# Performance work log

Hardware: AMD Instinct MI355X
Metric: run time of the kernel (lower is better)

Reference implementation:

```python
import jax, jax.numpy as jnp
import numpy as np

N_NODES = 100000
N_EDGES = 800000
NODE_IN = 32
EDGE_DIM = 84
HIDDEN = 24
HEAD_HIDDEN = 20
DEPTH = 2
CAT = 2 * HIDDEN + EDGE_DIM  # 132
LN_EPS = 1e-5


def _gelu(x):
    # torch nn.GELU default = exact erf form
    return jax.nn.gelu(x, approximate=False)


def _ln(x, g, b):
    m = jnp.mean(x, axis=-1, keepdims=True)
    v = jnp.var(x, axis=-1, keepdims=True)
    return (x - m) * jax.lax.rsqrt(v + LN_EPS) * g + b


def setup_inputs() -> dict:
    key = jax.random.key(0)
    ks = jax.random.split(key, 32)
    f = jnp.float32

    def nrm(k, shape, scale=0.05):
        return jax.random.normal(k, shape, dtype=f) * scale

    inp = {
        "x": jax.random.normal(ks[0], (N_NODES, NODE_IN), dtype=f),
        "edge_attr": jax.random.normal(ks[1], (N_EDGES, EDGE_DIM), dtype=f),
        # input projection
        "node_w": nrm(ks[2], (NODE_IN, HIDDEN)),
        "node_b": jnp.zeros((HIDDEN,), f),
        # intrinsic head
        "ih_w1": nrm(ks[3], (HIDDEN, HEAD_HIDDEN)),
        "ih_b1": jnp.zeros((HEAD_HIDDEN,), f),
        "ih_w2": nrm(ks[4], (HEAD_HIDDEN, 1)),
        "ih_b2": jnp.zeros((1,), f),
        # per-layer phi_e (stacked over depth)
        "pe_w1": nrm(ks[5], (DEPTH, CAT, EDGE_DIM)),
        "pe_b1": jnp.zeros((DEPTH, EDGE_DIM), f),
        "pe_w2": nrm(ks[6], (DEPTH, EDGE_DIM, EDGE_DIM)),
        "pe_b2": jnp.zeros((DEPTH, EDGE_DIM), f),
        # per-layer phi_v
        "pv_w1": nrm(ks[7], (DEPTH, CAT, HIDDEN)),
        "pv_b1": jnp.zeros((DEPTH, HIDDEN), f),
        "pv_w2": nrm(ks[8], (DEPTH, HIDDEN, HIDDEN)),
        "pv_b2": jnp.zeros((DEPTH, HIDDEN), f),
        # layer norms
        "ne_g": jnp.ones((DEPTH, EDGE_DIM), f),
        "ne_b": jnp.zeros((DEPTH, EDGE_DIM), f),
        "nv_g": jnp.ones((DEPTH, HIDDEN), f),
        "nv_b": jnp.zeros((DEPTH, HIDDEN), f),
        # context head
        "ch_w1": nrm(ks[9], (HIDDEN, HEAD_HIDDEN)),
        "ch_b1": jnp.zeros((HEAD_HIDDEN,), f),
        "ch_w2": nrm(ks[10], (HEAD_HIDDEN, 1)),
        "ch_b2": jnp.zeros((1,), f),
        "mu": jnp.zeros((), f),
        "edge_index": jax.random.randint(ks[11], (2, N_EDGES), 0, N_NODES),
    }
    return inp


def reference(x, edge_attr, node_w, node_b, ih_w1, ih_b1, ih_w2, ih_b2,
              pe_w1, pe_b1, pe_w2, pe_b2, pv_w1, pv_b1, pv_w2, pv_b2,
              ne_g, ne_b, nv_g, nv_b, ch_w1, ch_b1, ch_w2, ch_b2, mu,
              edge_index):
    src, dst = edge_index[0], edge_index[1]
    n = x.shape[0]
    # eval mode: dropout and edge_drop are inactive
    h = x @ node_w + node_b                                   # [N, H]
    intrinsic = (_gelu(h @ ih_w1 + ih_b1) @ ih_w2 + ih_b2)[:, 0]
    e = edge_attr                                             # [E, De]
    ones = jnp.ones((src.shape[0], 1), dtype=x.dtype)
    counts = jnp.maximum(jax.ops.segment_sum(ones, dst, num_segments=n), 1.0)
    for i in range(DEPTH):
        hs, hd = h[src], h[dst]                               # gathers [E, H]
        cat = jnp.concatenate([hs, hd, e], axis=-1)           # [E, 132]
        e_msg = _gelu(cat @ pe_w1[i] + pe_b1[i]) @ pe_w2[i] + pe_b2[i]
        e = _ln(e + e_msg, ne_g[i], ne_b[i])
        cat = jnp.concatenate([hs, hd, e], axis=-1)
        m = _gelu(cat @ pv_w1[i] + pv_b1[i]) @ pv_w2[i] + pv_b2[i]
        agg = jax.ops.segment_sum(m, dst, num_segments=n) / counts  # scatter-mean
        h = _ln(h + agg, nv_g[i], nv_b[i])
    context = (_gelu(h @ ch_w1 + ch_b1) @ ch_w2 + ch_b2)[:, 0]
    return mu + intrinsic + context
```

## Files before the change

### kernel.cpp

```cpp
#include <hip/hip_runtime.h>
#include <math.h>

#define N_NODES 100000
#define N_EDGES 800000
#define NODE_IN 32
#define EDGE_DIM 84
#define HIDDEN 24
#define HEAD_HIDDEN 20
#define CAT_DIM 132
#define LN_EPS 1e-5f

typedef __attribute__((ext_vector_type(8))) short short8;
typedef __attribute__((ext_vector_type(4))) short bfx4;
typedef __attribute__((ext_vector_type(4))) float f32x4;
typedef unsigned int uint;
typedef unsigned short ushort;

__device__ __forceinline__ float gelu_exact(float x) {
    return 0.5f * x * (1.0f + erff(x * 0.70710678118654752f));
}
__device__ __forceinline__ ushort f2bf(float f) {
    union { float f; uint u; } c; c.f = f;
    uint u = c.u;
    return (ushort)((u + 0x7fffu + ((u >> 16) & 1u)) >> 16);
}
__device__ __forceinline__ float bf2f(ushort s) {
    union { uint u; float f; } c; c.u = ((uint)s) << 16; return c.f;
}

__global__ void k_prep_w(const float* __restrict__ pe_w1, const float* __restrict__ pe_w2,
                         const float* __restrict__ pv_w1, const float* __restrict__ pv_w2,
                         ushort* __restrict__ wp) {
    int idx = blockIdx.x * 256 + threadIdx.x;
    int j = idx & 7;
    int lane = (idx >> 3) & 63;
    int frag = idx >> 9;
    int kq = (lane >> 4) * 8 + j;
    int n15 = lane & 15;
    float v = 0.f;
    if (frag < 60) {
        int l = frag / 30, f = frag % 30;
        int kt = f / 6, nt = f % 6;
        int k = kt * 32 + kq, n = nt * 16 + n15;
        if (k < CAT_DIM && n < EDGE_DIM) v = pe_w1[(l * CAT_DIM + k) * EDGE_DIM + n];
    } else if (frag < 96) {
        int f2 = frag - 60; int l = f2 / 18, f = f2 % 18;
        int kt = f / 6, nt = f % 6;
        int k = kt * 32 + kq, n = nt * 16 + n15;
        if (k < EDGE_DIM && n < EDGE_DIM) v = pe_w2[(l * EDGE_DIM + k) * EDGE_DIM + n];
    } else if (frag < 116) {
        int f2 = frag - 96; int l = f2 / 10, f = f2 % 10;
        int kt = f / 2, nt = f % 2;
        int k = kt * 32 + kq, n = nt * 16 + n15;
        if (k < CAT_DIM && n < HIDDEN) v = pv_w1[(l * CAT_DIM + k) * HIDDEN + n];
    } else {
        int f2 = frag - 116; int l = f2 / 2, nt = f2 % 2;
        int k = kq, n = nt * 16 + n15;
        if (k < HIDDEN && n < HIDDEN) v = pv_w2[(l * HIDDEN + k) * HIDDEN + n];
    }
    wp[idx] = f2bf(v);
}

__global__ void k_node_in(const float* __restrict__ x,
                          const float* __restrict__ node_w, const float* __restrict__ node_b,
                          const float* __restrict__ ih_w1, const float* __restrict__ ih_b1,
                          const float* __restrict__ ih_w2, const float* __restrict__ ih_b2,
                          float* __restrict__ h, ushort* __restrict__ h_bf,
                          float* __restrict__ intr) {
    int n = blockIdx.x * blockDim.x + threadIdx.x;
    if (n >= N_NODES) return;
    float xv[NODE_IN];
    const float4* xp = (const float4*)(x + (size_t)n * NODE_IN);
#pragma unroll
    for (int i = 0; i < NODE_IN / 4; i++) {
        float4 v = xp[i];
        xv[4*i+0] = v.x; xv[4*i+1] = v.y; xv[4*i+2] = v.z; xv[4*i+3] = v.w;
    }
    float hv[HIDDEN];
#pragma unroll
    for (int j = 0; j < HIDDEN; j++) hv[j] = node_b[j];
    for (int k = 0; k < NODE_IN; k++) {
        float xk = xv[k];
#pragma unroll
        for (int j = 0; j < HIDDEN; j++) hv[j] = fmaf(xk, node_w[k * HIDDEN + j], hv[j]);
    }
#pragma unroll
    for (int j = 0; j < HIDDEN; j++) {
        h[(size_t)n * HIDDEN + j] = hv[j];
        h_bf[(size_t)n * HIDDEN + j] = f2bf(hv[j]);
    }
    float acc = ih_b2[0];
    for (int j = 0; j < HEAD_HIDDEN; j++) {
        float t = ih_b1[j];
#pragma unroll
        for (int k = 0; k < HIDDEN; k++) t = fmaf(hv[k], ih_w1[k * HEAD_HIDDEN + j], t);
        acc = fmaf(gelu_exact(t), ih_w2[j], acc);
    }
    intr[n] = acc;
}

__global__ void k_counts(const int* __restrict__ ei, int* __restrict__ cnt) {
    int e = blockIdx.x * blockDim.x + threadIdx.x;
    if (e >= N_EDGES) return;
    atomicAdd(&cnt[ei[N_EDGES + e]], 1);
}

__global__ __launch_bounds__(256, 7)
void k_edge_fused(const ushort* __restrict__ h_bf,
                  const float* __restrict__ eattr,
                  ushort* __restrict__ e_bf,
                  const int* __restrict__ ei,
                  const ushort* __restrict__ w1f, const ushort* __restrict__ w2f,
                  const ushort* __restrict__ v1f, const ushort* __restrict__ v2f,
                  const float* __restrict__ b1, const float* __restrict__ b2,
                  const float* __restrict__ g, const float* __restrict__ bb,
                  const float* __restrict__ vb1, const float* __restrict__ vb2,
                  float* __restrict__ agg, int store_e) {
    __shared__ __align__(16) ushort sCat[64 * 136];

    const int tid = threadIdx.x;
    const int e0 = blockIdx.x * 64;
    const int lane = tid & 63, wave = tid >> 6;
    const int w16 = wave * 16;

#pragma unroll
    for (int i = 0; i < 2; i++) {
        int c = lane + 64 * i;
        if (c < 96) {
            int row_l = c / 6, part = c - row_l * 6;
            int row = w16 + row_l;
            int node = ei[(size_t)(part >= 3) * N_EDGES + e0 + row];
            short8 v = *(const short8*)(h_bf + (size_t)node * 24 + (part % 3) * 8);
            *(short8*)(sCat + row * 136 + part * 8) = v;
        }
    }
    if (eattr) {
#pragma unroll
        for (int i = 0; i < 6; i++) {
            int u = lane + 64 * i;
            if (u < 336) {
                int row_l = u / 21, c4 = u - row_l * 21;
                int row = w16 + row_l;
                f32x4 v = *(const f32x4*)(eattr + (size_t)(e0 + row) * 84 + c4 * 4);
                bfx4 wv;
                wv[0] = (short)f2bf(v[0]); wv[1] = (short)f2bf(v[1]);
                wv[2] = (short)f2bf(v[2]); wv[3] = (short)f2bf(v[3]);
                *(bfx4*)(sCat + row * 136 + 48 + c4 * 4) = wv;
            }
        }
        sCat[(w16 + (lane >> 2)) * 136 + 132 + (lane & 3)] = 0;
    } else {
#pragma unroll
        for (int i = 0; i < 3; i++) {
            int u = lane + 64 * i;
            if (u < 176) {
                int row_l = u / 11, c8 = u - row_l * 11;
                int row = w16 + row_l;
                *(short8*)(sCat + row * 136 + 48 + c8 * 8) =
                    *(const short8*)(e_bf + (size_t)(e0 + row) * 88 + c8 * 8);
            }
        }
    }

    const int quad = lane >> 4, l15 = lane & 15;
    const int cbase = quad * 8;
    const int rA = w16 + l15;

#pragma unroll
    for (int half = 0; half < 2; half++) {
        f32x4 acc[3];
#pragma unroll
        for (int n = 0; n < 3; n++) acc[n] = (f32x4)0.f;
#pragma unroll
        for (int kt = 0; kt < 5; kt++) {
            int c = kt * 32 + cbase; if (c > 128) c = 128;
            short8 a = *(const short8*)(sCat + rA * 136 + c);
            const short8* bp = (const short8*)w1f + kt * 6 * 64 + half * 3 * 64 + lane;
#pragma unroll
            for (int n = 0; n < 3; n++) {
                short8 b = bp[n * 64];
                acc[n] = __builtin_amdgcn_mfma_f32_16x16x32_bf16(a, b, acc[n], 0, 0, 0);
            }
        }
#pragma unroll
        for (int n = 0; n < 3; n++) {
            int col = (half * 3 + n) * 16 + l15;
            float bv = (col < EDGE_DIM) ? b1[col] : 0.f;
#pragma unroll
            for (int r = 0; r < 4; r++) {
                int row = w16 + quad * 4 + r;
                if (col < 88) sCat[row * 136 + 48 + col] = f2bf(gelu_exact(acc[n][r] + bv));
            }
        }
    }

    f32x4 acc2[6];
#pragma unroll
    for (int nt = 0; nt < 6; nt++) acc2[nt] = (f32x4)0.f;
#pragma unroll
    for (int kt = 0; kt < 3; kt++) {
        int c = kt * 32 + cbase; if (c > 80) c = 80;
        short8 a = *(const short8*)(sCat + rA * 136 + 48 + c);
        const short8* bp = (const short8*)w2f + kt * 6 * 64 + lane;
#pragma unroll
        for (int nt = 0; nt < 6; nt++) {
            short8 b = bp[nt * 64];
            acc2[nt] = __builtin_amdgcn_mfma_f32_16x16x32_bf16(a, b, acc2[nt], 0, 0, 0);
        }
    }

#pragma unroll
    for (int r = 0; r < 4; r++) {
        int row = w16 + quad * 4 + r;
        long rg = e0 + row;
        float vv[6];
        float ss = 0.f, qq = 0.f;
#pragma unroll
        for (int nt = 0; nt < 6; nt++) {
            int col = nt * 16 + l15;
            float v = 0.f;
            if (col < EDGE_DIM) {
                v = acc2[nt][r] + b2[col];
                v += eattr ? eattr[rg * 84 + col] : bf2f(e_bf[rg * 88 + col]);
            }
            vv[nt] = v; ss += v; qq = fmaf(v, v, qq);
        }
        ss += __shfl_xor(ss, 1); ss += __shfl_xor(ss, 2);
        ss += __shfl_xor(ss, 4); ss += __shfl_xor(ss, 8);
        qq += __shfl_xor(qq, 1); qq += __shfl_xor(qq, 2);
        qq += __shfl_xor(qq, 4); qq += __shfl_xor(qq, 8);
        float mean = ss * (1.f / EDGE_DIM);
        float var  = qq * (1.f / EDGE_DIM) - mean * mean;
        float rstd = rsqrtf(var + LN_EPS);
#pragma unroll
        for (int nt = 0; nt < 6; nt++) {
            int col = nt * 16 + l15;
            if (col < EDGE_DIM)
                sCat[row * 136 + 48 + col] = f2bf((vv[nt] - mean) * rstd * g[col] + bb[col]);
        }
    }

    f32x4 av[2];
#pragma unroll
    for (int nt = 0; nt < 2; nt++) av[nt] = (f32x4)0.f;
#pragma unroll
    for (int kt = 0; kt < 5; kt++) {
        int c = kt * 32 + cbase; if (c > 128) c = 128;
        short8 a = *(const short8*)(sCat + rA * 136 + c);
        const short8* bp = (const short8*)v1f + kt * 2 * 64 + lane;
#pragma unroll
        for (int nt = 0; nt < 2; nt++) {
            short8 b = bp[nt * 64];
            av[nt] = __builtin_amdgcn_mfma_f32_16x16x32_bf16(a, b, av[nt], 0, 0, 0);
        }
    }
#pragma unroll
    for (int nt = 0; nt < 2; nt++) {
        int col = nt * 16 + l15;
        float bv = (col < HIDDEN) ? vb1[col] : 0.f;
#pragma unroll
        for (int r = 0; r < 4; r++) {
            int row = w16 + quad * 4 + r;
            sCat[row * 136 + col] = f2bf(gelu_exact(av[nt][r] + bv));
        }
    }

    f32x4 av2[2];
#pragma unroll
    for (int nt = 0; nt < 2; nt++) av2[nt] = (f32x4)0.f;
    {
        short8 a = *(const short8*)(sCat + (size_t)rA * 136 + cbase);
        const short8* bp = (const short8*)v2f + lane;
#pragma unroll
        for (int nt = 0; nt < 2; nt++) {
            short8 b = bp[nt * 64];
            av2[nt] = __builtin_amdgcn_mfma_f32_16x16x32_bf16(a, b, av2[nt], 0, 0, 0);
        }
    }
    int dstv[4];
#pragma unroll
    for (int r = 0; r < 4; r++) dstv[r] = ei[(size_t)N_EDGES + e0 + w16 + quad * 4 + r];
#pragma unroll
    for (int nt = 0; nt < 2; nt++) {
        int col = nt * 16 + l15;
        if (col < HIDDEN) {
            float bv = vb2[col];
#pragma unroll
            for (int r = 0; r < 4; r++) {
                atomicAdd(&agg[(size_t)dstv[r] * HIDDEN + col], av2[nt][r] + bv);
            }
        }
    }

    if (store_e) {
        const uint* sU = (const uint*)sCat;
        uint* dst32 = (uint*)e_bf;
#pragma unroll
        for (int i = 0; i < 11; i++) {
            int idx = lane + 64 * i;
            int rl = idx / 44, d = idx - rl * 44;
            int row = w16 + rl;
            dst32[(size_t)(e0 + row) * 44 + d] = sU[row * 68 + 24 + d];
        }
    }
}

__global__ void k_node_up(float* __restrict__ h, ushort* __restrict__ h_bf,
                          const float* __restrict__ agg,
                          const int* __restrict__ cnt,
                          const float* __restrict__ g, const float* __restrict__ b) {
    int n = blockIdx.x * blockDim.x + threadIdx.x;
    if (n >= N_NODES) return;
    int c = cnt[n]; if (c < 1) c = 1;
    float inv = 1.0f / (float)c;
    float v[HIDDEN];
    float s = 0.f;
#pragma unroll
    for (int j = 0; j < HIDDEN; j++) {
        v[j] = h[(size_t)n * HIDDEN + j] + agg[(size_t)n * HIDDEN + j] * inv;
        s += v[j];
    }
    float mean = s * (1.f / HIDDEN);
    float sq = 0.f;
#pragma unroll
    for (int j = 0; j < HIDDEN; j++) { float d = v[j] - mean; sq = fmaf(d, d, sq); }
    float rstd = rsqrtf(sq * (1.f / HIDDEN) + LN_EPS);
#pragma unroll
    for (int j = 0; j < HIDDEN; j++) {
        float o = (v[j] - mean) * rstd * g[j] + b[j];
        h[(size_t)n * HIDDEN + j] = o;
        h_bf[(size_t)n * HIDDEN + j] = f2bf(o);
    }
}

__global__ void k_final(const float* __restrict__ h, const float* __restrict__ intr,
                        const float* __restrict__ ch_w1, const float* __restrict__ ch_b1,
                        const float* __restrict__ ch_w2, const float* __restrict__ ch_b2,
                        const float* __restrict__ mu, float* __restrict__ out) {
    int n = blockIdx.x * blockDim.x + threadIdx.x;
    if (n >= N_NODES) return;
    float hv[HIDDEN];
#pragma unroll
    for (int j = 0; j < HIDDEN; j++) hv[j] = h[(size_t)n * HIDDEN + j];
    float acc = ch_b2[0];
    for (int j = 0; j < HEAD_HIDDEN; j++) {
        float t = ch_b1[j];
#pragma unroll
        for (int k = 0; k < HIDDEN; k++) t = fmaf(hv[k], ch_w1[k * HEAD_HIDDEN + j], t);
        acc = fmaf(gelu_exact(t), ch_w2[j], acc);
    }
    out[n] = mu[0] + intr[n] + acc;
}

extern "C" void kernel_launch(void* const* d_in, const int* in_sizes, int n_in,
                              void* d_out, int out_size, void* d_ws, size_t ws_size,
                              hipStream_t stream) {
    const float* x        = (const float*)d_in[0];
    const float* edge_attr= (const float*)d_in[1];
    const float* node_w   = (const float*)d_in[2];
    const float* node_b   = (const float*)d_in[3];
    const float* ih_w1    = (const float*)d_in[4];
    const float* ih_b1    = (const float*)d_in[5];
    const float* ih_w2    = (const float*)d_in[6];
    const float* ih_b2    = (const float*)d_in[7];
    const float* pe_w1    = (const float*)d_in[8];
    const float* pe_b1    = (const float*)d_in[9];
    const float* pe_w2    = (const float*)d_in[10];
    const float* pe_b2    = (const float*)d_in[11];
    const float* pv_w1    = (const float*)d_in[12];
    const float* pv_b1    = (const float*)d_in[13];
    const float* pv_w2    = (const float*)d_in[14];
    const float* pv_b2    = (const float*)d_in[15];
    const float* ne_g     = (const float*)d_in[16];
    const float* ne_b     = (const float*)d_in[17];
    const float* nv_g     = (const float*)d_in[18];
    const float* nv_b     = (const float*)d_in[19];
    const float* ch_w1    = (const float*)d_in[20];
    const float* ch_b1    = (const float*)d_in[21];
    const float* ch_w2    = (const float*)d_in[22];
    const float* ch_b2    = (const float*)d_in[23];
    const float* mu       = (const float*)d_in[24];
    const int*   ei       = (const int*)d_in[25];

    char* ws = (char*)d_ws;
    float*  h    = (float*)ws;  ws += (size_t)N_NODES * HIDDEN * 4;
    float*  agg  = (float*)ws;  ws += (size_t)N_NODES * HIDDEN * 4;
    float*  intr = (float*)ws;  ws += (size_t)N_NODES * 4;
    int*    cnt  = (int*)ws;    ws += (size_t)N_NODES * 4;
    ushort* h_bf = (ushort*)ws; ws += (size_t)N_NODES * HIDDEN * 2;
    ushort* wp   = (ushort*)ws; ws += (size_t)61440 * 2;
    ws = (char*)(((size_t)ws + 255) & ~(size_t)255);
    ushort* e_bf = (ushort*)ws; ws += (size_t)N_EDGES * 88 * 2;

    const ushort* we1[2] = { wp + 0 * 15360, wp + 1 * 15360 };
    const ushort* we2[2] = { wp + 30720 + 0 * 9216, wp + 30720 + 1 * 9216 };
    const ushort* wv1[2] = { wp + 49152 + 0 * 5120, wp + 49152 + 1 * 5120 };
    const ushort* wv2[2] = { wp + 59392 + 0 * 1024, wp + 59392 + 1 * 1024 };

    hipMemsetAsync(cnt, 0, (size_t)N_NODES * 4, stream);
    k_prep_w<<<240, 256, 0, stream>>>(pe_w1, pe_w2, pv_w1, pv_w2, wp);
    k_counts<<<(N_EDGES + 255) / 256, 256, 0, stream>>>(ei, cnt);
    k_node_in<<<(N_NODES + 255) / 256, 256, 0, stream>>>(
        x, node_w, node_b, ih_w1, ih_b1, ih_w2, ih_b2, h, h_bf, intr);

    const int eb = N_EDGES / 64;
    for (int L = 0; L < 2; L++) {
        hipMemsetAsync(agg, 0, (size_t)N_NODES * HIDDEN * 4, stream);
        k_edge_fused<<<eb, 256, 0, stream>>>(
            h_bf, (L == 0) ? edge_attr : (const float*)nullptr, e_bf, ei,
            we1[L], we2[L], wv1[L], wv2[L],
            pe_b1 + (size_t)L * EDGE_DIM, pe_b2 + (size_t)L * EDGE_DIM,
            ne_g + (size_t)L * EDGE_DIM, ne_b + (size_t)L * EDGE_DIM,
            pv_b1 + (size_t)L * HIDDEN, pv_b2 + (size_t)L * HIDDEN,
            agg, (L == 0) ? 1 : 0);
        k_node_up<<<(N_NODES + 255) / 256, 256, 0, stream>>>(
            h, h_bf, agg, cnt, nv_g + (size_t)L * HIDDEN, nv_b + (size_t)L * HIDDEN);
    }
    k_final<<<(N_NODES + 255) / 256, 256, 0, stream>>>(
        h, intr, ch_w1, ch_b1, ch_w2, ch_b2, mu, (float*)d_out);
}
```

Measured before the change: 932.1 us.

## Preload edge residual into MFMA accumulators and merge first GEMM halves

Edge features are now loaded once, directly in the MFMA accumulator layout. They are written to LDS as bf16 for the GEMM input and kept in registers as the fp32 residual, which initialises acc2. This removes the second global read of edge_attr/e_bf in the LayerNorm epilogue. The first edge GEMM is now one pass with six accumulators instead of two halves of three, and launch bounds drop from 7 to 6 blocks per SM to allow the extra registers. The trade-offs are scalar rather than vectorised loads for the edge tile and possibly lower occupancy.

```diff
diff --git a/kernel.cpp b/kernel.cpp
--- a/kernel.cpp
+++ b/kernel.cpp
@@ -11,7 +11,6 @@
 #define LN_EPS 1e-5f
 
 typedef __attribute__((ext_vector_type(8))) short short8;
-typedef __attribute__((ext_vector_type(4))) short bfx4;
 typedef __attribute__((ext_vector_type(4))) float f32x4;
 typedef unsigned int uint;
 typedef unsigned short ushort;
@@ -105,7 +104,7 @@
     atomicAdd(&cnt[ei[N_EDGES + e]], 1);
 }
 
-__global__ __launch_bounds__(256, 7)
+__global__ __launch_bounds__(256, 6)
 void k_edge_fused(const ushort* __restrict__ h_bf,
                   const float* __restrict__ eattr,
                   ushort* __restrict__ e_bf,
@@ -122,6 +121,7 @@
     const int e0 = blockIdx.x * 64;
     const int lane = tid & 63, wave = tid >> 6;
     const int w16 = wave * 16;
+    const int quad = lane >> 4, l15 = lane & 15;
 
 #pragma unroll
     for (int i = 0; i < 2; i++) {
@@ -134,69 +134,58 @@
             *(short8*)(sCat + row * 136 + part * 8) = v;
         }
     }
-    if (eattr) {
-#pragma unroll
-        for (int i = 0; i < 6; i++) {
-            int u = lane + 64 * i;
-            if (u < 336) {
-                int row_l = u / 21, c4 = u - row_l * 21;
-                int row = w16 + row_l;
-                f32x4 v = *(const f32x4*)(eattr + (size_t)(e0 + row) * 84 + c4 * 4);
-                bfx4 wv;
-                wv[0] = (short)f2bf(v[0]); wv[1] = (short)f2bf(v[1]);
-                wv[2] = (short)f2bf(v[2]); wv[3] = (short)f2bf(v[3]);
-                *(bfx4*)(sCat + row * 136 + 48 + c4 * 4) = wv;
+
+    f32x4 acc2[6];
+#pragma unroll
+    for (int nt = 0; nt < 6; nt++) {
+        int col = nt * 16 + l15;
+#pragma unroll
+        for (int r = 0; r < 4; r++) {
+            int row = w16 + quad * 4 + r;
+            float v = 0.f;
+            if (eattr) {
+                if (col < EDGE_DIM) v = eattr[(size_t)(e0 + row) * 84 + col];
+                if (col < 88) sCat[row * 136 + 48 + col] = f2bf(v);
+            } else {
+                ushort u = 0;
+                if (col < 88) {
+                    u = e_bf[(size_t)(e0 + row) * 88 + col];
+                    sCat[row * 136 + 48 + col] = u;
+                }
+                v = bf2f(u);
             }
-        }
-        sCat[(w16 + (lane >> 2)) * 136 + 132 + (lane & 3)] = 0;
-    } else {
-#pragma unroll
-        for (int i = 0; i < 3; i++) {
-            int u = lane + 64 * i;
-            if (u < 176) {
-                int row_l = u / 11, c8 = u - row_l * 11;
-                int row = w16 + row_l;
-                *(short8*)(sCat + row * 136 + 48 + c8 * 8) =
-                    *(const short8*)(e_bf + (size_t)(e0 + row) * 88 + c8 * 8);
-            }
-        }
-    }
-
-    const int quad = lane >> 4, l15 = lane & 15;
+            acc2[nt][r] = v;
+        }
+    }
+
     const int cbase = quad * 8;
     const int rA = w16 + l15;
 
-#pragma unroll
-    for (int half = 0; half < 2; half++) {
-        f32x4 acc[3];
-#pragma unroll
-        for (int n = 0; n < 3; n++) acc[n] = (f32x4)0.f;
-#pragma unroll
-        for (int kt = 0; kt < 5; kt++) {
-            int c = kt * 32 + cbase; if (c > 128) c = 128;
-            short8 a = *(const short8*)(sCat + rA * 136 + c);
-            const short8* bp = (const short8*)w1f + kt * 6 * 64 + half * 3 * 64 + lane;
-#pragma unroll
-            for (int n = 0; n < 3; n++) {
-                short8 b = bp[n * 64];
-                acc[n] = __builtin_amdgcn_mfma_f32_16x16x32_bf16(a, b, acc[n], 0, 0, 0);
-            }
-        }
-#pragma unroll
-        for (int n = 0; n < 3; n++) {
-            int col = (half * 3 + n) * 16 + l15;
-            float bv = (col < EDGE_DIM) ? b1[col] : 0.f;
-#pragma unroll
-            for (int r = 0; r < 4; r++) {
-                int row = w16 + quad * 4 + r;
-                if (col < 88) sCat[row * 136 + 48 + col] = f2bf(gelu_exact(acc[n][r] + bv));
-            }
-        }
-    }
-
-    f32x4 acc2[6];
-#pragma unroll
-    for (int nt = 0; nt < 6; nt++) acc2[nt] = (f32x4)0.f;
+    f32x4 acc[6];
+#pragma unroll
+    for (int nt = 0; nt < 6; nt++) acc[nt] = (f32x4)0.f;
+#pragma unroll
+    for (int kt = 0; kt < 5; kt++) {
+        int c = kt * 32 + cbase; if (c > 128) c = 128;
+        short8 a = *(const short8*)(sCat + rA * 136 + c);
+        const short8* bp = (const short8*)w1f + kt * 6 * 64 + lane;
+#pragma unroll
+        for (int nt = 0; nt < 6; nt++) {
+            short8 b = bp[nt * 64];
+            acc[nt] = __builtin_amdgcn_mfma_f32_16x16x32_bf16(a, b, acc[nt], 0, 0, 0);
+        }
+    }
+#pragma unroll
+    for (int nt = 0; nt < 6; nt++) {
+        int col = nt * 16 + l15;
+        float bv = (col < EDGE_DIM) ? b1[col] : 0.f;
+#pragma unroll
+        for (int r = 0; r < 4; r++) {
+            int row = w16 + quad * 4 + r;
+            if (col < 88) sCat[row * 136 + 48 + col] = f2bf(gelu_exact(acc[nt][r] + bv));
+        }
+    }
+
 #pragma unroll
     for (int kt = 0; kt < 3; kt++) {
         int c = kt * 32 + cbase; if (c > 80) c = 80;
@@ -212,17 +201,12 @@
 #pragma unroll
     for (int r = 0; r < 4; r++) {
         int row = w16 + quad * 4 + r;
-        long rg = e0 + row;
         float vv[6];
         float ss = 0.f, qq = 0.f;
 #pragma unroll
         for (int nt = 0; nt < 6; nt++) {
             int col = nt * 16 + l15;
-            float v = 0.f;
-            if (col < EDGE_DIM) {
-                v = acc2[nt][r] + b2[col];
-                v += eattr ? eattr[rg * 84 + col] : bf2f(e_bf[rg * 88 + col]);
-            }
+            float v = (col < EDGE_DIM) ? (acc2[nt][r] + b2[col]) : 0.f;
             vv[nt] = v; ss += v; qq = fmaf(v, v, qq);
         }
         ss += __shfl_xor(ss, 1); ss += __shfl_xor(ss, 2);
```

After: 1.031 ms. 1.11x slower.
